# Kernel tuning notes

Measured on AMD Instinct MI355X. Metric: run time of the kernel, lower is better.

Reference implementation:

```python
import jax, jax.numpy as jnp
import numpy as np

VOCAB, EMBED, UNITS = 32000, 256, 1024


def setup_inputs() -> dict:
    key = jax.random.key(0)
    k1, k2, k3, k4, k5, k6 = jax.random.split(key, 6)
    B, S = 64, 512
    tokens = jax.random.randint(k1, (B, S), 0, VOCAB)
    emb = jax.random.uniform(k2, (VOCAB, EMBED), jnp.float32, -0.05, 0.05)
    # Keras GRU v2 (reset_after=True): kernel [E,3H], recurrent_kernel [H,3H], bias [2,3H]
    lim_k = np.sqrt(6.0 / (EMBED + 3 * UNITS)).astype(np.float32)
    lim_r = np.sqrt(6.0 / (UNITS + 3 * UNITS)).astype(np.float32)
    Wk = jax.random.uniform(k3, (EMBED, 3 * UNITS), jnp.float32, -lim_k, lim_k)
    Uk = jax.random.uniform(k4, (UNITS, 3 * UNITS), jnp.float32, -lim_r, lim_r)
    b = jnp.zeros((2, 3 * UNITS), jnp.float32)
    lim_o = np.sqrt(6.0 / (UNITS + VOCAB)).astype(np.float32)
    Wout = jax.random.uniform(k5, (UNITS, VOCAB), jnp.float32, -lim_o, lim_o)
    return {"tokens": tokens, "emb": emb, "Wk": Wk, "Uk": Uk, "b": b, "Wout": Wout}


def reference(tokens, emb, Wk, Uk, b, Wout):
    B, S = tokens.shape
    H = Uk.shape[0]
    x = emb[tokens]                      # [B,S,E] embedding lookup
    mask = tokens != 0                   # mask_zero=True
    # Precompute input projections for all timesteps: [B,S,3H]
    xproj = jnp.einsum('bse,eh->bsh', x, Wk) + b[0]
    xproj_t = jnp.transpose(xproj, (1, 0, 2))  # [S,B,3H]
    mask_t = mask.T                              # [S,B]

    def step(h, inp):
        xp, m = inp                      # xp: [B,3H], m: [B]
        rec = h @ Uk + b[1]              # [B,3H]
        xz, xr, xh = jnp.split(xp, 3, axis=-1)
        rz, rr, rh = jnp.split(rec, 3, axis=-1)
        z = jax.nn.sigmoid(xz + rz)
        r = jax.nn.sigmoid(xr + rr)
        hh = jnp.tanh(xh + r * rh)       # reset_after=True form
        h_new = z * h + (1.0 - z) * hh
        h_new = jnp.where(m[:, None], h_new, h)  # masked step: carry state
        return h_new, None

    h0 = jnp.zeros((B, H), x.dtype)
    hT, _ = jax.lax.scan(step, h0, (xproj_t, mask_t))
    return hT @ Wout                     # [B,VOCAB], no bias
```

## Files before the change

kernel.cpp:

```cpp
#include <hip/hip_runtime.h>
#include <cstddef>
#include <cstdint>

#define NB 64
#define NS 512
#define NE 256
#define NH 1024
#define NH3 3072
#define NV 32000

typedef unsigned short u16;
typedef unsigned int u32;
typedef unsigned long long u64;
typedef __attribute__((ext_vector_type(8))) short short8v;
typedef __attribute__((ext_vector_type(4))) float f32x4;

__device__ __forceinline__ u16 f2bf(float x) {
    u32 u = __float_as_uint(x);
    u32 r = (u + 0x7FFFu + ((u >> 16) & 1u)) >> 16;
    return (u16)r;
}
__device__ __forceinline__ float bf2f(u16 h) { return __uint_as_float(((u32)h) << 16); }

#define MFMA16(a, b, c) __builtin_amdgcn_mfma_f32_16x16x32_bf16((a), (b), (c), 0, 0, 0)

__global__ __launch_bounds__(256) void pack_uk(const float* __restrict__ Wk,
                                               const float* __restrict__ Uk,
                                               u16* __restrict__ Bh, u16* __restrict__ Bl) {
    const int idx = blockIdx.x * 256 + threadIdx.x;
    const int j = idx & 7;
    const int lane = (idx >> 3) & 63;
    const int slot = (idx >> 9) % 120;
    const int g = idx / (120 * 512);
    int tile, kc;
    if (slot < 40) { tile = 0; kc = slot; }
    else if (slot < 80) { tile = 1; kc = slot - 40; }
    else if (slot < 88) { tile = 2; kc = slot - 48; }
    else { tile = 3; kc = slot - 88; }
    const int k = kc * 32 + ((lane >> 4) << 3) + j;
    const int uu = g * 16 + (lane & 15);
    const int col = (tile == 0) ? uu : (tile == 1) ? (NH + uu) : (2 * NH + uu);
    const float v = (k < NH) ? Uk[(size_t)k * NH3 + col]
                             : Wk[(size_t)(k - NH) * NH3 + col];
    const u16 hi = f2bf(v);
    Bh[idx] = hi;
    Bl[idx] = f2bf(v - bf2f(hi));
}

__global__ __launch_bounds__(256) void pack_x(const int* __restrict__ tokens,
                                              const float* __restrict__ emb,
                                              u16* __restrict__ Xh, u16* __restrict__ Xl) {
    const int idx = blockIdx.x * 256 + threadIdx.x;
    const int j = idx & 7;
    const int lane = (idx >> 3) & 63;
    const int kcx = (idx >> 9) & 7;
    const int mg = (idx >> 12) & 3;
    const int s = idx >> 14;
    const int b = mg * 16 + (lane & 15);
    const int e = kcx * 32 + ((lane >> 4) << 3) + j;
    const int tok = tokens[b * NS + s];
    const float v = emb[(size_t)tok * NE + e];
    const u16 hi = f2bf(v);
    Xh[idx] = hi;
    Xl[idx] = f2bf(v - bf2f(hi));
}

__global__ __launch_bounds__(512, 2) void gru_scan(
    const int* __restrict__ tokens,
    const u16* __restrict__ Bh, const u16* __restrict__ Bl,
    const u16* __restrict__ Xh, const u16* __restrict__ Xl,
    const float* __restrict__ bias,
    float* __restrict__ hA,
    u16* __restrict__ sAh, u16* __restrict__ sAl,
    u16* __restrict__ sBh, u16* __restrict__ sBl,
    int* __restrict__ bar)
{
    __shared__ f32x4 red[8][4][64];
    __shared__ f32x4 preS[4][64];

    const int g = blockIdx.x & 63;
    const int mg = blockIdx.x >> 6;
    const int tid = threadIdx.x;
    const int w = tid >> 6;
    const int lane = tid & 63;
    const size_t laneo = (size_t)lane * 8;
    const size_t bbase = (size_t)g * 120 * 512;

    short8v Bz_h[5], Bz_l[5], Br_h[5], Br_l[5], B3_h[5], B3_l[5];
#pragma unroll
    for (int t = 0; t < 5; ++t) {
        const int kc = w + 8 * t;
        const size_t oz = bbase + (size_t)kc * 512 + laneo;
        const size_t orr = bbase + (size_t)(40 + kc) * 512 + laneo;
        const size_t o3 = bbase + (size_t)((t < 4) ? (88 + kc) : (48 + kc)) * 512 + laneo;
        Bz_h[t] = *(const short8v*)(Bh + oz);
        Bz_l[t] = *(const short8v*)(Bl + oz);
        Br_h[t] = *(const short8v*)(Bh + orr);
        Br_l[t] = *(const short8v*)(Bl + orr);
        B3_h[t] = *(const short8v*)(Bh + o3);
        B3_l[t] = *(const short8v*)(Bl + o3);
    }

    const int ll = tid & 63;
    const int q = tid >> 6;
    const int u = g * 16 + (ll & 15);
    const int brow = ((ll >> 4) << 2) + (q & 3);
    const int b = mg * 16 + brow;
    const float bz = bias[u] + bias[NH3 + u];
    const float br = bias[NH + u] + bias[NH3 + NH + u];
    const float bxh = bias[2 * NH + u];
    const float brh = bias[NH3 + 2 * NH + u];
    const size_t hoff = (size_t)b * NH + u;
    const size_t soA = (((size_t)mg * 32 + (u >> 5)) * 64 +
                        (brow + (((u & 31) >> 3) << 4))) * 8 + (u & 7);
    const int* tokp = tokens + b * NS;
    float hp = 0.0f;

    int* subp = bar + ((size_t)(mg * 8 + (g >> 3)) * 32);
    int* rootp = bar + 1024 + mg * 32;

    union AU { u64 q2[2]; short8v v; };

    for (int s = 0; s < NS; ++s) {
        const bool even = !(s & 1);
        const u16* hsh = even ? sAh : sBh;
        const u16* hsl = even ? sAl : sBl;
        u16* hnh = even ? sBh : sAh;
        u16* hnl = even ? sBl : sAl;

        asm volatile("" : "+v"(Bz_h[0]), "+v"(Bz_h[1]), "+v"(Bz_h[2]), "+v"(Bz_h[3]), "+v"(Bz_h[4]));
        asm volatile("" : "+v"(Bz_l[0]), "+v"(Bz_l[1]), "+v"(Bz_l[2]), "+v"(Bz_l[3]), "+v"(Bz_l[4]));
        asm volatile("" : "+v"(Br_h[0]), "+v"(Br_h[1]), "+v"(Br_h[2]), "+v"(Br_h[3]), "+v"(Br_h[4]));
        asm volatile("" : "+v"(Br_l[0]), "+v"(Br_l[1]), "+v"(Br_l[2]), "+v"(Br_l[3]), "+v"(Br_l[4]));
        asm volatile("" : "+v"(B3_h[0]), "+v"(B3_h[1]), "+v"(B3_h[2]), "+v"(B3_h[3]), "+v"(B3_h[4]));
        asm volatile("" : "+v"(B3_l[0]), "+v"(B3_l[1]), "+v"(B3_l[2]), "+v"(B3_l[3]), "+v"(B3_l[4]));

        f32x4 accz = {0.f, 0.f, 0.f, 0.f};
        f32x4 accr = accz, accxh = accz, accrh = accz;

#pragma unroll
        for (int t = 0; t < 5; ++t) {
            const int kc = w + 8 * t;
            short8v Ah, Al;
            if (t < 4) {
                const size_t aoff = ((size_t)(mg * 32 + kc) * 64) * 8 + laneo;
                AU ah, al;
                const u64* ph = (const u64*)(hsh + aoff);
                const u64* pl = (const u64*)(hsl + aoff);
                ah.q2[0] = __hip_atomic_load(ph + 0, __ATOMIC_RELAXED, __HIP_MEMORY_SCOPE_AGENT);
                ah.q2[1] = __hip_atomic_load(ph + 1, __ATOMIC_RELAXED, __HIP_MEMORY_SCOPE_AGENT);
                al.q2[0] = __hip_atomic_load(pl + 0, __ATOMIC_RELAXED, __HIP_MEMORY_SCOPE_AGENT);
                al.q2[1] = __hip_atomic_load(pl + 1, __ATOMIC_RELAXED, __HIP_MEMORY_SCOPE_AGENT);
                Ah = ah.v; Al = al.v;
            } else {
                const size_t aoff = ((((size_t)s * 4 + mg) * 8 + (kc - 32)) * 64) * 8 + laneo;
                Ah = *(const short8v*)(Xh + aoff);
                Al = *(const short8v*)(Xl + aoff);
            }
            accz = MFMA16(Ah, Bz_h[t], accz);
            accr = MFMA16(Ah, Br_h[t], accr);
            if (t < 4) {
                accrh = MFMA16(Ah, B3_h[t], accrh);
                accrh = MFMA16(Al, B3_h[t], accrh);
                accrh = MFMA16(Ah, B3_l[t], accrh);
            } else {
                accxh = MFMA16(Ah, B3_h[t], accxh);
                accxh = MFMA16(Al, B3_h[t], accxh);
                accxh = MFMA16(Ah, B3_l[t], accxh);
            }
            accz = MFMA16(Al, Bz_h[t], accz);
            accz = MFMA16(Ah, Bz_l[t], accz);
            accr = MFMA16(Al, Br_h[t], accr);
            accr = MFMA16(Ah, Br_l[t], accr);
        }

        red[w][0][lane] = accz;
        red[w][1][lane] = accr;
        red[w][2][lane] = accxh;
        red[w][3][lane] = accrh;
        __syncthreads();

        if (tid < 256) {
            f32x4 sum = red[0][q][ll];
#pragma unroll
            for (int w2 = 1; w2 < 8; ++w2) {
                const f32x4 v = red[w2][q][ll];
                sum.x += v.x; sum.y += v.y; sum.z += v.z; sum.w += v.w;
            }
            preS[q][ll] = sum;
        }
        __syncthreads();

        if (tid < 256) {
            const float pz = ((const float*)&preS[0][ll])[q];
            const float pr = ((const float*)&preS[1][ll])[q];
            const float pxh = ((const float*)&preS[2][ll])[q];
            const float prh = ((const float*)&preS[3][ll])[q];
            const float z = 1.0f / (1.0f + expf(-(pz + bz)));
            const float r = 1.0f / (1.0f + expf(-(pr + br)));
            const float hh = tanhf(pxh + bxh + r * (prh + brh));
            const bool m = tokp[s] != 0;
            const float hnv = m ? (z * hp + (1.0f - z) * hh) : hp;
            hp = hnv;
            if (s < NS - 1) {
                const u16 hi = f2bf(hnv);
                const u16 lo = f2bf(hnv - bf2f(hi));
                __hip_atomic_store(hnh + soA, hi, __ATOMIC_RELAXED, __HIP_MEMORY_SCOPE_AGENT);
                __hip_atomic_store(hnl + soA, lo, __ATOMIC_RELAXED, __HIP_MEMORY_SCOPE_AGENT);
            }
        }

        if (s < NS - 1) {
            __syncthreads();
            if (tid == 0) {
                const int v = __hip_atomic_fetch_add(subp, 1, __ATOMIC_RELAXED,
                                                     __HIP_MEMORY_SCOPE_AGENT);
                if ((v & 7) == 7) {
                    __hip_atomic_fetch_add(rootp, 1, __ATOMIC_RELAXED,
                                           __HIP_MEMORY_SCOPE_AGENT);
                }
                const int tgt = 8 * (s + 1);
                while (__hip_atomic_load(rootp, __ATOMIC_RELAXED,
                                         __HIP_MEMORY_SCOPE_AGENT) < tgt) {
                    __builtin_amdgcn_s_sleep(1);
                }
            }
            __syncthreads();
        }
    }

    if (tid < 256) hA[hoff] = hp;
}

__global__ __launch_bounds__(256) void out_mm2(const float* __restrict__ h,
                                               const float* __restrict__ Wout,
                                               float* __restrict__ out) {
    __shared__ float red[4][NB][64];
    const int cl = threadIdx.x & 63;
    const int ks = threadIdx.x >> 6;
    const int col = blockIdx.x * 64 + cl;
    float acc[NB];
#pragma unroll
    for (int b = 0; b < NB; ++b) acc[b] = 0.0f;
    const int k0 = ks * 256;
    for (int k = k0; k < k0 + 256; ++k) {
        const float wv = Wout[(size_t)k * NV + col];
#pragma unroll
        for (int b = 0; b < NB; ++b) acc[b] = fmaf(h[b * NH + k], wv, acc[b]);
    }
#pragma unroll
    for (int b = 0; b < NB; ++b) red[ks][b][cl] = acc[b];
    __syncthreads();
    for (int i = threadIdx.x; i < NB * 64; i += 256) {
        const int b = i >> 6;
        const int c2 = i & 63;
        const float v = red[0][b][c2] + red[1][b][c2] + red[2][b][c2] + red[3][b][c2];
        out[(size_t)b * NV + blockIdx.x * 64 + c2] = v;
    }
}

#define NBT 8
#define UT 16
#define KS 16
#define KH (NH / KS)
#define KX (NE / KS)
__device__ __forceinline__ int hrow(int k) { return k + (k >> 6); }
__device__ __forceinline__ int xrow(int k) { return k + (k >> 4); }

__global__ __launch_bounds__(256) void gru_step2(
    const int* __restrict__ tokens, const float* __restrict__ emb,
    const float* __restrict__ Wk, const float* __restrict__ Uk,
    const float* __restrict__ bias,
    const float* __restrict__ h_in, float* __restrict__ h_out, int s)
{
    __shared__ float hs[NH + NH / 64][NBT];
    __shared__ float xs[NE + NE / 16][NBT];
    __shared__ float red[4][NBT][256];
    const int tid = threadIdx.x;
    const int ug = blockIdx.x & 63;
    const int bg = blockIdx.x >> 6;
    for (int i = tid; i < NBT * (NE / 4); i += 256) {
        const int bl = i >> 6; const int e4 = i & 63;
        const int b = bg * NBT + bl;
        const int tok = tokens[b * NS + s];
        const float4 v = ((const float4*)(emb + (size_t)tok * NE))[e4];
        const int k0 = e4 * 4;
        xs[xrow(k0 + 0)][bl] = v.x; xs[xrow(k0 + 1)][bl] = v.y;
        xs[xrow(k0 + 2)][bl] = v.z; xs[xrow(k0 + 3)][bl] = v.w;
    }
    for (int i = tid; i < NBT * (NH / 4); i += 256) {
        const int bl = i >> 8; const int k4 = i & 255;
        const int b = bg * NBT + bl;
        const float4 v = ((const float4*)(h_in + (size_t)b * NH))[k4];
        const int r = hrow(k4 * 4);
        hs[r + 0][bl] = v.x; hs[r + 1][bl] = v.y; hs[r + 2][bl] = v.z; hs[r + 3][bl] = v.w;
    }
    __syncthreads();
    const int ul = tid & 15;
    const int ks = tid >> 4;
    const int u = ug * UT + ul;
    float az[NBT], ar[NBT], axh[NBT], arh[NBT];
#pragma unroll
    for (int b = 0; b < NBT; ++b) { az[b] = 0.f; ar[b] = 0.f; axh[b] = 0.f; arh[b] = 0.f; }
    {
        size_t off = (size_t)(ks * KH) * NH3 + u;
        const int r0 = ks * (KH + 1);
#pragma unroll 4
        for (int kk = 0; kk < KH; ++kk) {
            const float uz = Uk[off], ur = Uk[off + NH], uh = Uk[off + 2 * NH];
            float hv[8];
            *(float4*)&hv[0] = *(const float4*)&hs[r0 + kk][0];
            *(float4*)&hv[4] = *(const float4*)&hs[r0 + kk][4];
#pragma unroll
            for (int b = 0; b < NBT; ++b) {
                az[b] = fmaf(hv[b], uz, az[b]); ar[b] = fmaf(hv[b], ur, ar[b]);
                arh[b] = fmaf(hv[b], uh, arh[b]);
            }
            off += NH3;
        }
    }
    {
        size_t off = (size_t)(ks * KX) * NH3 + u;
        const int r0 = ks * (KX + 1);
#pragma unroll 4
        for (int kk = 0; kk < KX; ++kk) {
            const float wz = Wk[off], wr = Wk[off + NH], wh = Wk[off + 2 * NH];
            float xv[8];
            *(float4*)&xv[0] = *(const float4*)&xs[r0 + kk][0];
            *(float4*)&xv[4] = *(const float4*)&xs[r0 + kk][4];
#pragma unroll
            for (int b = 0; b < NBT; ++b) {
                az[b] = fmaf(xv[b], wz, az[b]); ar[b] = fmaf(xv[b], wr, ar[b]);
                axh[b] = fmaf(xv[b], wh, axh[b]);
            }
            off += NH3;
        }
    }
#pragma unroll
    for (int b = 0; b < NBT; ++b) {
        red[0][b][tid] = az[b]; red[1][b][tid] = ar[b];
        red[2][b][tid] = axh[b]; red[3][b][tid] = arh[b];
    }
    __syncthreads();
    if (tid < 128) {
        const int ul2 = tid & 15;
        const int bl = tid >> 4;
        const int u2 = ug * UT + ul2;
        const int b = bg * NBT + bl;
        float sz = 0.f, sr = 0.f, sxh = 0.f, srh = 0.f;
#pragma unroll
        for (int k2 = 0; k2 < KS; ++k2) {
            const int t2 = k2 * 16 + ul2;
            sz += red[0][bl][t2]; sr += red[1][bl][t2];
            sxh += red[2][bl][t2]; srh += red[3][bl][t2];
        }
        sz += bias[u2] + bias[NH3 + u2];
        sr += bias[NH + u2] + bias[NH3 + NH + u2];
        sxh += bias[2 * NH + u2];
        srh += bias[NH3 + 2 * NH + u2];
        const float z = 1.0f / (1.0f + expf(-sz));
        const float r = 1.0f / (1.0f + expf(-sr));
        const float hh = tanhf(sxh + r * srh);
        const float hp = hs[hrow(u2)][bl];
        const bool m = tokens[b * NS + s] != 0;
        h_out[(size_t)b * NH + u2] = m ? (z * hp + (1.0f - z) * hh) : hp;
    }
}

extern "C" void kernel_launch(void* const* d_in, const int* in_sizes, int n_in,
                              void* d_out, int out_size, void* d_ws, size_t ws_size,
                              hipStream_t stream) {
    const int* tokens = (const int*)d_in[0];
    const float* emb = (const float*)d_in[1];
    const float* Wk = (const float*)d_in[2];
    const float* Uk = (const float*)d_in[3];
    const float* bias = (const float*)d_in[4];
    const float* Wout = (const float*)d_in[5];
    float* out = (float*)d_out;

    const size_t B_ELEMS = (size_t)64 * 120 * 512;
    const size_t X_ELEMS = (size_t)NS * 4 * 8 * 512;
    const size_t H_ELEMS = (size_t)NB * NH;
    const size_t HS_ELEMS = (size_t)4 * 32 * 64 * 8;

    size_t off = 0;
    auto take = [&](size_t bytes) { size_t o = off; off += (bytes + 255) & ~255ULL; return o; };
    const size_t oBh = take(B_ELEMS * 2), oBl = take(B_ELEMS * 2);
    const size_t oXh = take(X_ELEMS * 2), oXl = take(X_ELEMS * 2);
    const size_t ohA = take(H_ELEMS * 4);
    const size_t osAh = take(HS_ELEMS * 2), osAl = take(HS_ELEMS * 2);
    const size_t osBh = take(HS_ELEMS * 2), osBl = take(HS_ELEMS * 2);
    const size_t obar = take(1152 * 4);

    char* base = (char*)d_ws;

    if (off <= ws_size) {
        u16* Bh = (u16*)(base + oBh); u16* Bl = (u16*)(base + oBl);
        u16* Xh = (u16*)(base + oXh); u16* Xl = (u16*)(base + oXl);
        float* hA = (float*)(base + ohA);
        u16* sAh = (u16*)(base + osAh); u16* sAl = (u16*)(base + osAl);
        u16* sBh = (u16*)(base + osBh); u16* sBl = (u16*)(base + osBl);
        int* bar = (int*)(base + obar);

        hipMemsetAsync(sAh, 0, HS_ELEMS * 2, stream);
        hipMemsetAsync(sAl, 0, HS_ELEMS * 2, stream);
        hipMemsetAsync(bar, 0, 1152 * 4, stream);
        pack_uk<<<(int)(B_ELEMS / 256), 256, 0, stream>>>(Wk, Uk, Bh, Bl);
        pack_x<<<(int)(X_ELEMS / 256), 256, 0, stream>>>(tokens, emb, Xh, Xl);

        gru_scan<<<256, 512, 0, stream>>>(tokens, Bh, Bl, Xh, Xl, bias,
                                          hA, sAh, sAl, sBh, sBl, bar);
        out_mm2<<<500, 256, 0, stream>>>(hA, Wout, out);
    } else {
        float* h0 = (float*)d_ws;
        float* h1 = h0 + H_ELEMS;
        hipMemsetAsync(h0, 0, H_ELEMS * 4, stream);
        for (int s = 0; s < NS; ++s) {
            const float* hin = (s & 1) ? h1 : h0;
            float* hout = (s & 1) ? h0 : h1;
            gru_step2<<<512, 256, 0, stream>>>(tokens, emb, Wk, Uk, bias, hin, hout, s);
        }
        out_mm2<<<500, 256, 0, stream>>>(h0, Wout, out);
    }
}
```

Measured before the change: 2.825 ms.

## Replace hierarchical atomic barrier with per-block step flags and packed hidden state

The two-level fetch-add grid barrier is replaced by per-block step-counter flags. Wave 0 of each block polls all 256 flags with wide loads at the start of the next step, and the trailing __syncthreads is dropped. Hidden-state hi/lo bf16 halves are packed into one u32 store and one set of loads, and the input-projection X tile and the mask are loaded before the wait. The recurrent MFMAs are split across two accumulator sets for more instruction-level parallelism. The goal is lower per-step synchronisation latency and fewer memory transactions, at the cost of more polling traffic and reliance on relaxed-ordering visibility.

```diff
diff --git a/kernel.cpp b/kernel.cpp
--- a/kernel.cpp
+++ b/kernel.cpp
@@ -71,9 +71,8 @@
     const u16* __restrict__ Xh, const u16* __restrict__ Xl,
     const float* __restrict__ bias,
     float* __restrict__ hA,
-    u16* __restrict__ sAh, u16* __restrict__ sAl,
-    u16* __restrict__ sBh, u16* __restrict__ sBl,
-    int* __restrict__ bar)
+    u32* __restrict__ sA, u32* __restrict__ sB,
+    int* __restrict__ flags)
 {
     __shared__ f32x4 red[8][4][64];
     __shared__ f32x4 preS[4][64];
@@ -116,17 +115,45 @@
     const int* tokp = tokens + b * NS;
     float hp = 0.0f;
 
-    int* subp = bar + ((size_t)(mg * 8 + (g >> 3)) * 32);
-    int* rootp = bar + 1024 + mg * 32;
-
-    union AU { u64 q2[2]; short8v v; };
-
     for (int s = 0; s < NS; ++s) {
-        const bool even = !(s & 1);
-        const u16* hsh = even ? sAh : sBh;
-        const u16* hsl = even ? sAl : sBl;
-        u16* hnh = even ? sBh : sAh;
-        u16* hnl = even ? sBl : sAl;
+        const u32* scur = (s & 1) ? sB : sA;
+        u32* snext = (s & 1) ? sA : sB;
+
+        const size_t xoff = ((((size_t)s * 4 + mg) * 8 + w) * 64) * 8 + laneo;
+        const short8v XAh = *(const short8v*)(Xh + xoff);
+        const short8v XAl = *(const short8v*)(Xl + xoff);
+        const bool m = tokp[s] != 0;
+
+        if (s > 0) {
+            if (w == 0) {
+                const u64* fp = (const u64*)flags + (size_t)lane * 2;
+                for (;;) {
+                    const u64 q0 = __hip_atomic_load(fp + 0, __ATOMIC_RELAXED,
+                                                     __HIP_MEMORY_SCOPE_AGENT);
+                    const u64 q1 = __hip_atomic_load(fp + 1, __ATOMIC_RELAXED,
+                                                     __HIP_MEMORY_SCOPE_AGENT);
+                    int mn = (int)q0;
+                    const int a1 = (int)(q0 >> 32), b0 = (int)q1, b1 = (int)(q1 >> 32);
+                    mn = mn < a1 ? mn : a1;
+                    mn = mn < b0 ? mn : b0;
+                    mn = mn < b1 ? mn : b1;
+                    if (__all(mn >= s)) break;
+                    __builtin_amdgcn_s_sleep(1);
+                }
+            }
+            __syncthreads();
+        }
+
+        u64 qf[4][4];
+#pragma unroll
+        for (int t = 0; t < 4; ++t) {
+            const int kc = w + 8 * t;
+            const u64* p = (const u64*)(scur + (((size_t)(mg * 32 + kc)) << 9) + laneo);
+            qf[t][0] = __hip_atomic_load(p + 0, __ATOMIC_RELAXED, __HIP_MEMORY_SCOPE_AGENT);
+            qf[t][1] = __hip_atomic_load(p + 1, __ATOMIC_RELAXED, __HIP_MEMORY_SCOPE_AGENT);
+            qf[t][2] = __hip_atomic_load(p + 2, __ATOMIC_RELAXED, __HIP_MEMORY_SCOPE_AGENT);
+            qf[t][3] = __hip_atomic_load(p + 3, __ATOMIC_RELAXED, __HIP_MEMORY_SCOPE_AGENT);
+        }
 
         asm volatile("" : "+v"(Bz_h[0]), "+v"(Bz_h[1]), "+v"(Bz_h[2]), "+v"(Bz_h[3]), "+v"(Bz_h[4]));
         asm volatile("" : "+v"(Bz_l[0]), "+v"(Bz_l[1]), "+v"(Bz_l[2]), "+v"(Bz_l[3]), "+v"(Bz_l[4]));
@@ -135,49 +162,58 @@
         asm volatile("" : "+v"(B3_h[0]), "+v"(B3_h[1]), "+v"(B3_h[2]), "+v"(B3_h[3]), "+v"(B3_h[4]));
         asm volatile("" : "+v"(B3_l[0]), "+v"(B3_l[1]), "+v"(B3_l[2]), "+v"(B3_l[3]), "+v"(B3_l[4]));
 
-        f32x4 accz = {0.f, 0.f, 0.f, 0.f};
-        f32x4 accr = accz, accxh = accz, accrh = accz;
-
-#pragma unroll
-        for (int t = 0; t < 5; ++t) {
-            const int kc = w + 8 * t;
-            short8v Ah, Al;
-            if (t < 4) {
-                const size_t aoff = ((size_t)(mg * 32 + kc) * 64) * 8 + laneo;
-                AU ah, al;
-                const u64* ph = (const u64*)(hsh + aoff);
-                const u64* pl = (const u64*)(hsl + aoff);
-                ah.q2[0] = __hip_atomic_load(ph + 0, __ATOMIC_RELAXED, __HIP_MEMORY_SCOPE_AGENT);
-                ah.q2[1] = __hip_atomic_load(ph + 1, __ATOMIC_RELAXED, __HIP_MEMORY_SCOPE_AGENT);
-                al.q2[0] = __hip_atomic_load(pl + 0, __ATOMIC_RELAXED, __HIP_MEMORY_SCOPE_AGENT);
-                al.q2[1] = __hip_atomic_load(pl + 1, __ATOMIC_RELAXED, __HIP_MEMORY_SCOPE_AGENT);
-                Ah = ah.v; Al = al.v;
+        f32x4 az0 = {0.f, 0.f, 0.f, 0.f};
+        f32x4 az1 = az0, ar0 = az0, ar1 = az0, ah0 = az0, ah1 = az0, axh = az0;
+
+#pragma unroll
+        for (int t = 0; t < 4; ++t) {
+            union { u32 uw[4]; short8v v; } Ahv, Alv;
+#pragma unroll
+            for (int k = 0; k < 2; ++k) {
+                const u32 c0 = (u32)qf[t][2 * k],     c1 = (u32)(qf[t][2 * k] >> 32);
+                const u32 c2 = (u32)qf[t][2 * k + 1], c3 = (u32)(qf[t][2 * k + 1] >> 32);
+                Ahv.uw[2 * k]     = (c0 & 0xffffu) | (c1 << 16);
+                Ahv.uw[2 * k + 1] = (c2 & 0xffffu) | (c3 << 16);
+                Alv.uw[2 * k]     = (c0 >> 16) | (c1 & 0xffff0000u);
+                Alv.uw[2 * k + 1] = (c2 >> 16) | (c3 & 0xffff0000u);
+            }
+            const short8v Ah = Ahv.v, Al = Alv.v;
+            if (t & 1) {
+                az1 = MFMA16(Ah, Bz_h[t], az1);
+                ar1 = MFMA16(Ah, Br_h[t], ar1);
+                ah1 = MFMA16(Ah, B3_h[t], ah1);
+                ah1 = MFMA16(Al, B3_h[t], ah1);
+                ah1 = MFMA16(Ah, B3_l[t], ah1);
+                az1 = MFMA16(Al, Bz_h[t], az1);
+                az1 = MFMA16(Ah, Bz_l[t], az1);
+                ar1 = MFMA16(Al, Br_h[t], ar1);
+                ar1 = MFMA16(Ah, Br_l[t], ar1);
             } else {
-                const size_t aoff = ((((size_t)s * 4 + mg) * 8 + (kc - 32)) * 64) * 8 + laneo;
-                Ah = *(const short8v*)(Xh + aoff);
-                Al = *(const short8v*)(Xl + aoff);
-            }
-            accz = MFMA16(Ah, Bz_h[t], accz);
-            accr = MFMA16(Ah, Br_h[t], accr);
-            if (t < 4) {
-                accrh = MFMA16(Ah, B3_h[t], accrh);
-                accrh = MFMA16(Al, B3_h[t], accrh);
-                accrh = MFMA16(Ah, B3_l[t], accrh);
-            } else {
-                accxh = MFMA16(Ah, B3_h[t], accxh);
-                accxh = MFMA16(Al, B3_h[t], accxh);
-                accxh = MFMA16(Ah, B3_l[t], accxh);
-            }
-            accz = MFMA16(Al, Bz_h[t], accz);
-            accz = MFMA16(Ah, Bz_l[t], accz);
-            accr = MFMA16(Al, Br_h[t], accr);
-            accr = MFMA16(Ah, Br_l[t], accr);
-        }
-
-        red[w][0][lane] = accz;
-        red[w][1][lane] = accr;
-        red[w][2][lane] = accxh;
-        red[w][3][lane] = accrh;
+                az0 = MFMA16(Ah, Bz_h[t], az0);
+                ar0 = MFMA16(Ah, Br_h[t], ar0);
+                ah0 = MFMA16(Ah, B3_h[t], ah0);
+                ah0 = MFMA16(Al, B3_h[t], ah0);
+                ah0 = MFMA16(Ah, B3_l[t], ah0);
+                az0 = MFMA16(Al, Bz_h[t], az0);
+                az0 = MFMA16(Ah, Bz_l[t], az0);
+                ar0 = MFMA16(Al, Br_h[t], ar0);
+                ar0 = MFMA16(Ah, Br_l[t], ar0);
+            }
+        }
+        az1 = MFMA16(XAh, Bz_h[4], az1);
+        ar1 = MFMA16(XAh, Br_h[4], ar1);
+        axh = MFMA16(XAh, B3_h[4], axh);
+        axh = MFMA16(XAl, B3_h[4], axh);
+        axh = MFMA16(XAh, B3_l[4], axh);
+        az1 = MFMA16(XAl, Bz_h[4], az1);
+        az1 = MFMA16(XAh, Bz_l[4], az1);
+        ar1 = MFMA16(XAl, Br_h[4], ar1);
+        ar1 = MFMA16(XAh, Br_l[4], ar1);
+
+        red[w][0][lane] = az0 + az1;
+        red[w][1][lane] = ar0 + ar1;
+        red[w][2][lane] = axh;
+        red[w][3][lane] = ah0 + ah1;
         __syncthreads();
 
         if (tid < 256) {
@@ -199,33 +235,22 @@
             const float z = 1.0f / (1.0f + expf(-(pz + bz)));
             const float r = 1.0f / (1.0f + expf(-(pr + br)));
             const float hh = tanhf(pxh + bxh + r * (prh + brh));
-            const bool m = tokp[s] != 0;
             const float hnv = m ? (z * hp + (1.0f - z) * hh) : hp;
             hp = hnv;
             if (s < NS - 1) {
                 const u16 hi = f2bf(hnv);
                 const u16 lo = f2bf(hnv - bf2f(hi));
-                __hip_atomic_store(hnh + soA, hi, __ATOMIC_RELAXED, __HIP_MEMORY_SCOPE_AGENT);
-                __hip_atomic_store(hnl + soA, lo, __ATOMIC_RELAXED, __HIP_MEMORY_SCOPE_AGENT);
+                __hip_atomic_store(snext + soA, (u32)hi | ((u32)lo << 16),
+                                   __ATOMIC_RELAXED, __HIP_MEMORY_SCOPE_AGENT);
             }
         }
 
         if (s < NS - 1) {
             __syncthreads();
             if (tid == 0) {
-                const int v = __hip_atomic_fetch_add(subp, 1, __ATOMIC_RELAXED,
-                                                     __HIP_MEMORY_SCOPE_AGENT);
-                if ((v & 7) == 7) {
-                    __hip_atomic_fetch_add(rootp, 1, __ATOMIC_RELAXED,
-                                           __HIP_MEMORY_SCOPE_AGENT);
-                }
-                const int tgt = 8 * (s + 1);
-                while (__hip_atomic_load(rootp, __ATOMIC_RELAXED,
-                                         __HIP_MEMORY_SCOPE_AGENT) < tgt) {
-                    __builtin_amdgcn_s_sleep(1);
-                }
-            }
-            __syncthreads();
+                __hip_atomic_store(flags + blockIdx.x, s + 1,
+                                   __ATOMIC_RELAXED, __HIP_MEMORY_SCOPE_AGENT);
+            }
         }
     }
 
@@ -388,9 +413,8 @@
     const size_t oBh = take(B_ELEMS * 2), oBl = take(B_ELEMS * 2);
     const size_t oXh = take(X_ELEMS * 2), oXl = take(X_ELEMS * 2);
     const size_t ohA = take(H_ELEMS * 4);
-    const size_t osAh = take(HS_ELEMS * 2), osAl = take(HS_ELEMS * 2);
-    const size_t osBh = take(HS_ELEMS * 2), osBl = take(HS_ELEMS * 2);
-    const size_t obar = take(1152 * 4);
+    const size_t osA = take(HS_ELEMS * 4), osB = take(HS_ELEMS * 4);
+    const size_t oflag = take(256 * 4);
 
     char* base = (char*)d_ws;
 
@@ -398,18 +422,16 @@
         u16* Bh = (u16*)(base + oBh); u16* Bl = (u16*)(base + oBl);
         u16* Xh = (u16*)(base + oXh); u16* Xl = (u16*)(base + oXl);
         float* hA = (float*)(base + ohA);
-        u16* sAh = (u16*)(base + osAh); u16* sAl = (u16*)(base + osAl);
-        u16* sBh = (u16*)(base + osBh); u16* sBl = (u16*)(base + osBl);
-        int* bar = (int*)(base + obar);
-
-        hipMemsetAsync(sAh, 0, HS_ELEMS * 2, stream);
-        hipMemsetAsync(sAl, 0, HS_ELEMS * 2, stream);
-        hipMemsetAsync(bar, 0, 1152 * 4, stream);
+        u32* sA = (u32*)(base + osA); u32* sB = (u32*)(base + osB);
+        int* flags = (int*)(base + oflag);
+
+        hipMemsetAsync(sA, 0, HS_ELEMS * 4, stream);
+        hipMemsetAsync(flags, 0, 256 * 4, stream);
         pack_uk<<<(int)(B_ELEMS / 256), 256, 0, stream>>>(Wk, Uk, Bh, Bl);
         pack_x<<<(int)(X_ELEMS / 256), 256, 0, stream>>>(tokens, emb, Xh, Xl);
 
         gru_scan<<<256, 512, 0, stream>>>(tokens, Bh, Bl, Xh, Xl, bias,
-                                          hA, sAh, sAl, sBh, sBl, bar);
+                                          hA, sA, sB, flags);
         out_mm2<<<500, 256, 0, stream>>>(hA, Wout, out);
     } else {
         float* h0 = (float*)d_ws;
```

After: 4.058 ms. 43.6% more time.
